# Optimization experiments

Measured on AMD Instinct MI355X. Metric: run time of the kernel, lower is better.

The kernel has to match this reference:

```python
import jax, jax.numpy as jnp
import numpy as np

NUM_SPLITS = 4
SPLIT_CH = 4          # 16 channels / 4 splits
N_BRANCH = NUM_SPLITS * 2   # 2 pyramid branches per group
K = 2                 # multi_frequency_compression k
MAX_U, MAX_V = 5, 5
N_CLASSES = 60
LN_EPS = 1e-5


def _conv(x, w):
    # x: [B, Cin, H, W], w: [Cout, Cin, kh, kw], SAME padding, stride 1
    return jax.lax.conv_general_dilated(
        x, w, window_strides=(1, 1), padding='SAME',
        dimension_numbers=('NCHW', 'OIHW', 'NCHW'))


def _branch(x, w3, b3, w5, b5, w7, b7):
    # one PyramidMultiScaleCNN branch: dense 3x3 -> 5x5 -> 7x7 with input re-concat
    a = jax.nn.relu(_conv(x, w3) + b3[None, :, None, None])            # [B,64,H,W]
    b = jax.nn.relu(_conv(jnp.concatenate([a, x], 1), w5) + b5[None, :, None, None])  # [B,128,H,W]
    c = jax.nn.relu(_conv(jnp.concatenate([b, x], 1), w7) + b7[None, :, None, None])  # [B,256,H,W]
    return jnp.concatenate([a, b, c], axis=1)                          # [B,448,H,W]


def _dct_basis(H, W, dtype):
    # first K frequency pairs (u,v) in row-major order of a MAX_U x MAX_V grid
    uv = [(i // MAX_V, i % MAX_V) for i in range(K)]
    u = jnp.array([p[0] for p in uv], dtype=dtype)   # [K]
    v = jnp.array([p[1] for p in uv], dtype=dtype)   # [K]
    h = jnp.arange(H, dtype=dtype) + 0.5
    w = jnp.arange(W, dtype=dtype) + 0.5
    cos_u = jnp.cos(jnp.pi * u[:, None] * h[None, :] / H)  # [K,H]
    cos_v = jnp.cos(jnp.pi * v[:, None] * w[None, :] / W)  # [K,W]
    return cos_u, cos_v


def setup_inputs() -> dict:
    key = jax.random.key(0)
    ks = jax.random.split(key, 16)
    B, C, H, W = 16, 16, 32, 32
    s = 0.02
    x = jax.random.normal(ks[0], (B, C, H, W), jnp.float32)
    # stacked params for the 8 identical-shaped pyramid branches (index = 2*group + branch)
    w3 = jax.random.normal(ks[1], (N_BRANCH, 64, SPLIT_CH, 3, 3), jnp.float32) * s
    b3 = jnp.zeros((N_BRANCH, 64), jnp.float32)
    w5 = jax.random.normal(ks[2], (N_BRANCH, 128, 64 + SPLIT_CH, 5, 5), jnp.float32) * s
    b5 = jnp.zeros((N_BRANCH, 128), jnp.float32)
    w7 = jax.random.normal(ks[3], (N_BRANCH, 256, 128 + SPLIT_CH, 7, 7), jnp.float32) * s
    b7 = jnp.zeros((N_BRANCH, 256), jnp.float32)
    fused_c = N_BRANCH * 448  # 3584
    Wg = jax.random.normal(ks[4], (N_CLASSES, fused_c), jnp.float32) * s
    bg = jnp.zeros((N_CLASSES,), jnp.float32)
    f_dct = fused_c * K       # 7168
    gamma = jnp.ones((f_dct,), jnp.float32)
    beta = jnp.zeros((f_dct,), jnp.float32)
    Wd = jax.random.normal(ks[5], (N_CLASSES, f_dct), jnp.float32) * s
    bd = jnp.zeros((N_CLASSES,), jnp.float32)
    return {"x": x, "w3": w3, "b3": b3, "w5": w5, "b5": b5, "w7": w7, "b7": b7,
            "Wg": Wg, "bg": bg, "gamma": gamma, "beta": beta, "Wd": Wd, "bd": bd}


def reference(x, w3, b3, w5, b5, w7, b7, Wg, bg, gamma, beta, Wd, bd):
    B, C, H, W = x.shape
    # split channels into groups: [NUM_SPLITS, B, SPLIT_CH, H, W]
    parts = x.reshape(B, NUM_SPLITS, SPLIT_CH, H, W).transpose(1, 0, 2, 3, 4)
    # each group feeds 2 branches; branch index i = 2*group + branch matches fused cat order
    xg = jnp.repeat(parts, 2, axis=0)                               # [8,B,SPLIT_CH,H,W]
    outs = jax.vmap(_branch)(xg, w3, b3, w5, b5, w7, b7)            # [8,B,448,H,W]
    fused = outs.transpose(1, 0, 2, 3, 4).reshape(B, N_BRANCH * 448, H, W)  # [B,3584,H,W]

    # GAP head
    gap_feat = fused.mean(axis=(2, 3))                              # [B,3584]
    gap_pred = gap_feat @ Wg.T + bg                                 # [B,60]

    # batched multi-frequency DCT compression (replaces per-sample Python loop)
    cos_u, cos_v = _dct_basis(H, W, fused.dtype)                    # [K,H],[K,W]
    dct = jnp.einsum('bchw,kh,kw->bck', fused, cos_u, cos_v)        # [B,3584,K]
    dct = dct.reshape(B, -1)                                        # [B,7168]

    mu = dct.mean(axis=-1, keepdims=True)
    var = jnp.var(dct, axis=-1, keepdims=True)
    normed = (dct - mu) * jax.lax.rsqrt(var + LN_EPS) * gamma + beta
    # dropout omitted (eval mode)
    dct_pred = normed @ Wd.T + bd                                   # [B,60]
    return (gap_pred, dct_pred)
```

## Files before the change

kernel.cpp:

```cpp
#include <hip/hip_runtime.h>
#include <math.h>

#define PI_F 3.14159265358979323846f

typedef short bf16x8 __attribute__((ext_vector_type(8)));
typedef float f32x4  __attribute__((ext_vector_type(4)));
typedef float f32x16 __attribute__((ext_vector_type(16)));

__device__ __forceinline__ short f2bf(float f) {
    union { float f; unsigned u; } v; v.f = f;
    unsigned r = v.u + 0x7fffu + ((v.u >> 16) & 1u);
    return (short)(r >> 16);
}

__device__ __forceinline__ void gld16(const short* g, short* l) {
    __builtin_amdgcn_global_load_lds(
        (const __attribute__((address_space(1))) unsigned int*)g,
        (__attribute__((address_space(3))) unsigned int*)l, 16, 0, 0);
}


__global__ __launch_bounds__(256) void prep_s1in(const float* __restrict__ x, short* __restrict__ dst) {
    int idx = blockIdx.x * 256 + threadIdx.x;
    if (idx >= 64 * 1024) return;
    int px = idx & 1023;
    int g  = (idx >> 10) & 3;
    int b  = idx >> 12;
    short v8[8];
    #pragma unroll
    for (int j = 0; j < 8; ++j) {
        float f = (j < 4) ? x[((b * 16 + g * 4 + j) << 10) + px] : 0.f;
        v8[j] = f2bf(f);
    }
    *(int4*)(dst + (size_t)idx * 8) = *(const int4*)v8;
}

__global__ __launch_bounds__(256) void prep_sx(const float* __restrict__ x, short* __restrict__ dst,
                                               int CHS, int CH0) {
    int idx = blockIdx.x * 256 + threadIdx.x;
    if (idx >= 128 * 1024) return;
    int px = idx & 1023, pair = idx >> 10;
    int i = pair >> 4, b = pair & 15, g = i >> 1;
    short v8[8];
    #pragma unroll
    for (int j = 0; j < 8; ++j) {
        float f = (j < 4) ? x[((b * 16 + g * 4 + j) << 10) + px] : 0.f;
        v8[j] = f2bf(f);
    }
    *(int4*)(dst + (size_t)idx * CHS + CH0) = *(const int4*)v8;
}

__global__ __launch_bounds__(256) void prep_s3x(const float* __restrict__ x, short* __restrict__ dst) {
    int idx = blockIdx.x * 256 + threadIdx.x;
    if (idx >= 128 * 1024) return;
    int px = idx & 1023, pair = idx >> 10;
    int i = pair >> 4, b = pair & 15, g = i >> 1;
    int R = px >> 5, C = px & 31;
    short v8[8];
    #pragma unroll
    for (int j = 0; j < 8; ++j) {
        float f = (j < 4) ? x[((b * 16 + g * 4 + j) << 10) + px] : 0.f;
        v8[j] = f2bf(f);
    }
    int p = ((C + 3) * 136 + 128) * 2;
    p ^= ((p >> 7) & 1) << 4;
    *(int4*)((char*)dst + ((size_t)pair * 38 + R + 3) * 11264 + p) = *(const int4*)v8;
}

template<int KS, int CHS, int CINR, int COUT, int NCH>
__global__ __launch_bounds__(256) void wprep_d(const float* __restrict__ w, short* __restrict__ Bw) {
    constexpr int TOTAL = 8 * KS * NCH * COUT * 4;
    int idx = blockIdx.x * 256 + threadIdx.x;
    if (idx >= TOTAL) return;
    int kb = idx & 3;
    int r  = idx >> 2;
    int n  = r % COUT;  r /= COUT;
    int c  = r % NCH;   r /= NCH;
    int kh = r % KS;
    int br = r / KS;
    short v8[8];
    #pragma unroll
    for (int j = 0; j < 8; ++j) {
        int k   = c * 32 + kb * 8 + j;
        int kwc = k / CHS;
        int ch  = k - kwc * CHS;
        float f = (kwc < KS && ch < CINR)
                ? w[(((size_t)br * COUT + n) * CINR + ch) * (KS * KS) + kh * KS + kwc] : 0.f;
        v8[j] = f2bf(f);
    }
    *(int4*)(Bw + (size_t)idx * 8) = *(const int4*)v8;
}

__global__ __launch_bounds__(256) void wprep7c(const float* __restrict__ w, short* __restrict__ Bw) {
    __shared__ float lds[12936];
    const int t = threadIdx.x;
    const int pairN = blockIdx.x & 127;
    const int br    = blockIdx.x >> 7;
    const int n0 = pairN * 2;
    const float* src = w + ((size_t)br * 256 + n0) * 6468;
    for (int e = t; e < 3234; e += 256)
        *(float4*)(lds + e * 4) = *(const float4*)(src + e * 4);
    __syncthreads();
    for (int e = t; e < 1680; e += 256) {
        int oct = e & 3;
        int r = e >> 2;
        int c  = r % 30; r /= 30;
        int kh = r % 7;
        int dn = r / 7;
        short v8[8];
        #pragma unroll
        for (int j = 0; j < 8; ++j) {
            int k = c * 32 + oct * 8 + j;
            int kwc = k / 136, ch = k - kwc * 136;
            float f = (kwc < 7 && ch < 132) ? lds[dn * 6468 + ch * 49 + kh * 7 + kwc] : 0.f;
            v8[j] = f2bf(f);
        }
        size_t dst = ((((size_t)br * 7 + kh) * 30 + c) * 256 + (n0 + dn)) * 32 + oct * 8;
        *(int4*)(Bw + dst) = *(const int4*)v8;
    }
}

template<int KS, int CHS, int COUT, int CHS_OUT, int FOFF, bool S1SRC, bool POUT>
__global__ __launch_bounds__(512, 2) void conv_hk(
    const short* __restrict__ sIn,
    short* __restrict__ sOut,
    const short* __restrict__ Bw,
    const float* __restrict__ bias,
    float* __restrict__ sums)
{
    constexpr int PAD    = KS / 2;
    constexpr int NCH    = (KS * CHS + 31) / 32;
    constexpr int TCX    = 32 + (NCH * 32 - 1) / CHS;
    constexpr int NSLOT  = 9;
    constexpr int NFN    = COUT / 64;
    constexpr int CPP    = CHS / 8;
    constexpr int RCHK   = TCX * CPP;
    constexpr int CHUNKB = COUT * 32;
    static_assert(NCH == 1 || (NCH % 2) == 0, "NCH must be 1 or even");
    static_assert(RCHK <= 512, "single stg reg");

    __shared__ int4 AtileV[(NSLOT * TCX * CHS) / 8];
    short* Atile = (short*)AtileV;

    const int t    = threadIdx.x;
    const int lane = t & 63, w = t >> 6;
    const int wm = w >> 2, wn = w & 3;
    const int lm = lane & 15, kb = lane >> 4;

    const int bid = blockIdx.x;
    const int i  = bid & 7;
    const int b  = (bid >> 3) & 15;
    const int mt = bid >> 7;
    const int r0 = mt * 8;

    const int pairIdx = i * 16 + b;
    const int pairPx = pairIdx << 10;
    const int srcPx  = S1SRC ? ((b * 4 + (i >> 1)) << 10) : pairPx;

    int nIdx[NFN], nOff[NFN];
    #pragma unroll
    for (int fn = 0; fn < NFN; ++fn) {
        nIdx[fn] = wn * (COUT / 4) + fn * 16 + lm;
        nOff[fn] = nIdx[fn] * 32 + kb * 8;
    }

    f32x4 acc[8][NFN];
    #pragma unroll
    for (int fm = 0; fm < 8; ++fm)
        #pragma unroll
        for (int fn = 0; fn < NFN; ++fn)
            acc[fm][fn] = (f32x4){0.f, 0.f, 0.f, 0.f};

    const short* Bp = Bw + (size_t)i * KS * NCH * CHUNKB;
    bf16x8 b0[NFN], b1[NFN];
    #pragma unroll
    for (int fn = 0; fn < NFN; ++fn)
        b0[fn] = *(const bf16x8*)(Bp + nOff[fn]);

    for (int e = t; e < 9 * RCHK; e += 512) {
        int j  = e / RCHK, e2 = e - j * RCHK;
        int tc = e2 / CPP, kc = e2 - tc * CPP;
        int rin = r0 - PAD + j, cin = tc - PAD;
        int4 v = {0, 0, 0, 0};
        if (rin >= 0 && rin < 32 && cin >= 0 && cin < 32)
            v = *(const int4*)(sIn + (size_t)(srcPx + rin * 32 + cin) * CHS + kc * 8);
        *(int4*)(Atile + (j * TCX + tc) * CHS + kc * 8) = v;
    }
    __syncthreads();

    int aB[8];

    for (int kh = 0; kh < KS; ++kh) {
        #pragma unroll
        for (int fm = 0; fm < 8; ++fm) {
            int slot = kh + wm * 4 + (fm >> 1);
            if (slot >= NSLOT) slot -= NSLOT;
            aB[fm] = (slot * TCX + (fm & 1) * 16 + lm) * CHS + kb * 8;
        }

        const bool doStage = (kh <= KS - 3);
        const int stRin = r0 - PAD + kh + 9;
        int4 stg0 = {0, 0, 0, 0};
        if (doStage) {
            if (t < RCHK) {
                int tc = t / CPP, kc = t - tc * CPP;
                int cin = tc - PAD;
                if (stRin >= 0 && stRin < 32 && cin >= 0 && cin < 32)
                    stg0 = *(const int4*)(sIn + (size_t)(srcPx + stRin * 32 + cin) * CHS + kc * 8);
            }
        }

        if constexpr (NCH == 1) {
            __builtin_amdgcn_s_setprio(1);
            #pragma unroll
            for (int fm = 0; fm < 8; ++fm) {
                bf16x8 af = *(const bf16x8*)(Atile + aB[fm]);
                #pragma unroll
                for (int fn = 0; fn < NFN; ++fn)
                    acc[fm][fn] = __builtin_amdgcn_mfma_f32_16x16x32_bf16(af, b0[fn], acc[fm][fn], 0, 0, 0);
            }
            __builtin_amdgcn_s_setprio(0);
            if (kh < KS - 1) {
                #pragma unroll
                for (int fn = 0; fn < NFN; ++fn)
                    b0[fn] = *(const bf16x8*)(Bp + CHUNKB + nOff[fn]);
            }
            Bp += CHUNKB;
        } else {
            #pragma unroll 1
            for (int c = 0; c < NCH; c += 2) {
                #pragma unroll
                for (int fn = 0; fn < NFN; ++fn)
                    b1[fn] = *(const bf16x8*)(Bp + (size_t)(c + 1) * CHUNKB + nOff[fn]);
                __builtin_amdgcn_s_setprio(1);
                #pragma unroll
                for (int fm = 0; fm < 8; ++fm) {
                    bf16x8 af = *(const bf16x8*)(Atile + aB[fm] + c * 32);
                    #pragma unroll
                    for (int fn = 0; fn < NFN; ++fn)
                        acc[fm][fn] = __builtin_amdgcn_mfma_f32_16x16x32_bf16(af, b0[fn], acc[fm][fn], 0, 0, 0);
                }
                __builtin_amdgcn_s_setprio(0);
                if (!(kh == KS - 1 && c + 2 >= NCH)) {
                    #pragma unroll
                    for (int fn = 0; fn < NFN; ++fn)
                        b0[fn] = *(const bf16x8*)(Bp + (size_t)(c + 2) * CHUNKB + nOff[fn]);
                }
                __builtin_amdgcn_s_setprio(1);
                #pragma unroll
                for (int fm = 0; fm < 8; ++fm) {
                    bf16x8 af = *(const bf16x8*)(Atile + aB[fm] + (c + 1) * 32);
                    #pragma unroll
                    for (int fn = 0; fn < NFN; ++fn)
                        acc[fm][fn] = __builtin_amdgcn_mfma_f32_16x16x32_bf16(af, b1[fn], acc[fm][fn], 0, 0, 0);
                }
                __builtin_amdgcn_s_setprio(0);
            }
            Bp += (size_t)NCH * CHUNKB;
        }

        __syncthreads();
        if (doStage && t < RCHK) {
            int tc = t / CPP, kc = t - tc * CPP;
            *(int4*)(Atile + (kh * TCX + tc) * CHS + kc * 8) = stg0;
        }
    }

    float cwv[2][4];
    #pragma unroll
    for (int half = 0; half < 2; ++half)
        #pragma unroll
        for (int r = 0; r < 4; ++r)
            cwv[half][r] = cosf(PI_F * (half * 16 + kb * 4 + r + 0.5f) / 32.f);

    #pragma unroll
    for (int fn = 0; fn < NFN; ++fn) {
        int n = nIdx[fn];
        float bv = bias[i * COUT + n];
        float s0 = 0.f, s1 = 0.f;
        #pragma unroll
        for (int fm = 0; fm < 8; ++fm) {
            int imgrow = wm * 4 + (fm >> 1);
            int half = fm & 1;
            #pragma unroll
            for (int r = 0; r < 4; ++r) {
                float v = fmaxf(acc[fm][fn][r] + bv, 0.f);
                int col = half * 16 + kb * 4 + r;
                int R = r0 + imgrow;
                if constexpr (POUT) {
                    int p = ((col + 3) * CHS_OUT + n) * 2;
                    p ^= ((p >> 7) & 1) << 4;
                    *(short*)((char*)sOut + ((size_t)pairIdx * 38 + R + 3) * 11264 + p) = f2bf(v);
                } else if constexpr (CHS_OUT > 0) {
                    sOut[(size_t)(pairPx + R * 32 + col) * CHS_OUT + n] = f2bf(v);
                }
                s0 += v;
                s1 += v * cwv[half][r];
            }
        }
        s0 += __shfl_xor(s0, 16); s1 += __shfl_xor(s1, 16);
        s0 += __shfl_xor(s0, 32); s1 += __shfl_xor(s1, 32);
        if (kb == 0) {
            int ch = i * 448 + FOFF + n;
            atomicAdd(&sums[((size_t)b * 3584 + ch) * 2 + 0], s0);
            atomicAdd(&sums[((size_t)b * 3584 + ch) * 2 + 1], s1);
        }
    }
}

__global__ __launch_bounds__(512, 2) void conv7_fused(
    const short* __restrict__ sPad,
    const short* __restrict__ Bw,
    const float* __restrict__ bias,
    float* __restrict__ sums)
{
    constexpr int NCH = 30, COUT = 256;
    constexpr int RSTR = 5632;
    constexpr int CHUNKB = COUT * 32;

    __shared__ int4 AldsV[(14 * RSTR) / 8];
    short* Alds = (short*)AldsV;

    const int t    = threadIdx.x;
    const int lane = t & 63, w = t >> 6;
    const int ln = lane & 31, hi = lane >> 5;

    const int bid = blockIdx.x;
    const int i  = bid & 7;
    const int b  = (bid >> 3) & 15;
    const int mt = bid >> 7;
    const int r0 = mt * 8;
    const size_t sBase = (size_t)(i * 16 + b) * 38 * RSTR;

    const int n = w * 32 + ln;
    const int nOffB = n * 32 + hi * 8;
    const int cstart = (w & 4) ? 15 : 0;

    f32x16 acc[8];
    #pragma unroll
    for (int ro = 0; ro < 8; ++ro) acc[ro] = (f32x16)(0.f);

    const short* BpI = Bw + (size_t)i * 7 * NCH * CHUNKB;

    for (int s = w; s < 154; s += 8) {
        int j = s / 11, sg = s - j * 11;
        gld16(sPad + sBase + (size_t)(r0 + j) * RSTR + sg * 512 + lane * 8,
              Alds + j * RSTR + sg * 512 + lane * 8);
    }
    bf16x8 bA[7], bB[7];
    #pragma unroll
    for (int kh = 0; kh < 7; ++kh)
        bA[kh] = *(const bf16x8*)(BpI + ((size_t)kh * NCH + cstart) * CHUNKB + nOffB);
    __syncthreads();

    auto HALF = [&](bf16x8 (&bq)[7], int c, int kk) {
        int swb = ln * 272 + c * 64 + kk * 32 + hi * 16;
        swb ^= ((swb >> 7) & 1) << 4;
        __builtin_amdgcn_s_setprio(1);
        #pragma unroll
        for (int j = 0; j < 14; ++j) {
            bf16x8 af = *(const bf16x8*)((const char*)Alds + j * 11264 + swb);
            const int klo = (j > 7) ? (j - 7) : 0;
            const int khi = (j < 6) ? j : 6;
            #pragma unroll
            for (int kh = klo; kh <= khi; ++kh)
                acc[j - kh] = __builtin_amdgcn_mfma_f32_32x32x16_bf16(af, bq[kh], acc[j - kh], 0, 0, 0);
        }
        __builtin_amdgcn_s_setprio(0);
    };

    #pragma unroll 1
    for (int ci = 0; ci < NCH; ++ci) {
        int cc = cstart + ci; if (cc >= NCH) cc -= NCH;
        int cn = cc + 1;      if (cn >= NCH) cn -= NCH;
        #pragma unroll
        for (int kh = 0; kh < 7; ++kh)
            bB[kh] = *(const bf16x8*)(BpI + ((size_t)kh * NCH + cc) * CHUNKB + nOffB + 16);
        HALF(bA, cc, 0);
        if (ci + 1 < NCH) {
            #pragma unroll
            for (int kh = 0; kh < 7; ++kh)
                bA[kh] = *(const bf16x8*)(BpI + ((size_t)kh * NCH + cn) * CHUNKB + nOffB);
        }
        HALF(bB, cc, 1);
    }

    float cw[16];
    #pragma unroll
    for (int r = 0; r < 16; ++r) {
        int px = (r & 3) + 8 * (r >> 2) + 4 * hi;
        cw[r] = cosf(PI_F * (px + 0.5f) / 32.f);
    }

    float bv = bias[i * COUT + n];
    float s0 = 0.f, s1 = 0.f;
    #pragma unroll
    for (int ro = 0; ro < 8; ++ro) {
        #pragma unroll
        for (int r = 0; r < 16; ++r) {
            float v = fmaxf(acc[ro][r] + bv, 0.f);
            s0 += v;
            s1 += v * cw[r];
        }
    }
    s0 += __shfl_xor(s0, 32);
    s1 += __shfl_xor(s1, 32);
    if (hi == 0) {
        int ch = i * 448 + 192 + n;
        atomicAdd(&sums[((size_t)b * 3584 + ch) * 2 + 0], s0);
        atomicAdd(&sums[((size_t)b * 3584 + ch) * 2 + 1], s1);
    }
}

__global__ __launch_bounds__(256) void ln_stats(const float* __restrict__ sums,
                                                float* __restrict__ stats) {
    __shared__ float red[8];
    const int b = blockIdx.x;
    const int t = threadIdx.x, lane = t & 63, wv = t >> 6;
    const float* S = sums + (size_t)b * 7168;
    float ls = 0.f, lq = 0.f;
    for (int f = t; f < 7168; f += 256) { float v = S[f]; ls += v; lq += v * v; }
    for (int m = 1; m < 64; m <<= 1) { ls += __shfl_xor(ls, m); lq += __shfl_xor(lq, m); }
    if (lane == 0) { red[wv] = ls; red[4 + wv] = lq; }
    __syncthreads();
    if (t == 0) {
        float ts = red[0] + red[1] + red[2] + red[3];
        float tq = red[4] + red[5] + red[6] + red[7];
        float mu  = ts * (1.f / 7168.f);
        float var = tq * (1.f / 7168.f) - mu * mu;
        stats[b * 2 + 0] = mu;
        stats[b * 2 + 1] = rsqrtf(var + 1e-5f);
    }
}

__global__ __launch_bounds__(256) void head_gemv(
    const float* __restrict__ sums,
    const float* __restrict__ stats,
    const float* __restrict__ Wg, const float* __restrict__ bg,
    const float* __restrict__ gamma, const float* __restrict__ beta,
    const float* __restrict__ Wd, const float* __restrict__ bd,
    float* __restrict__ out)
{
    __shared__ float red[8];
    const int n = blockIdx.x % 60;
    const int b = blockIdx.x / 60;
    const int t = threadIdx.x, lane = t & 63, wv = t >> 6;
    const float* S  = sums + (size_t)b * 7168;
    const float mu  = stats[b * 2 + 0];
    const float inv = stats[b * 2 + 1];

    const float* wd = Wd + (size_t)n * 7168;
    float accd = 0.f;
    for (int f = t; f < 7168; f += 256) {
        float v = (S[f] - mu) * inv * gamma[f] + beta[f];
        accd = fmaf(v, wd[f], accd);
    }
    const float* wg = Wg + (size_t)n * 3584;
    float accg = 0.f;
    for (int ch = t; ch < 3584; ch += 256)
        accg = fmaf(S[2 * ch], wg[ch], accg);

    for (int m = 1; m < 64; m <<= 1) { accg += __shfl_xor(accg, m); accd += __shfl_xor(accd, m); }
    if (lane == 0) { red[wv] = accg; red[4 + wv] = accd; }
    __syncthreads();
    if (t == 0) {
        float g = red[0] + red[1] + red[2] + red[3];
        float d = red[4] + red[5] + red[6] + red[7];
        out[b * 60 + n]       = g * (1.f / 1024.f) + bg[n];
        out[960 + b * 60 + n] = d + bd[n];
    }
}

extern "C" void kernel_launch(void* const* d_in, const int* in_sizes, int n_in,
                              void* d_out, int out_size, void* d_ws, size_t ws_size,
                              hipStream_t stream)
{
    const float* x     = (const float*)d_in[0];
    const float* w3    = (const float*)d_in[1];
    const float* b3    = (const float*)d_in[2];
    const float* w5    = (const float*)d_in[3];
    const float* b5    = (const float*)d_in[4];
    const float* w7    = (const float*)d_in[5];
    const float* b7    = (const float*)d_in[6];
    const float* Wg    = (const float*)d_in[7];
    const float* bg    = (const float*)d_in[8];
    const float* gamma = (const float*)d_in[9];
    const float* beta  = (const float*)d_in[10];
    const float* Wd    = (const float*)d_in[11];
    const float* bd    = (const float*)d_in[12];
    float* out = (float*)d_out;

    char* p = (char*)d_ws;
    float* sums  = (float*)p;             p += 458752;
    float* stats = (float*)p;             p += 128;
    short* s1in  = (short*)p;             p += 1048576;
    short* s2in  = (short*)p;             p += 18874368;
    short* s3pad = (short*)p;             p += 54788096;
    short* Bw3   = (short*)p;             p += 98304;
    short* Bw5   = (short*)p;             p += 3932160;
    short* Bw7   = (short*)p;             p += 27525120;

    hipMemsetAsync(sums, 0, 458752, stream);
    hipMemsetAsync(s3pad, 0, 54788096, stream);
    prep_s1in<<<dim3(256), dim3(256), 0, stream>>>(x, s1in);
    prep_sx<<<dim3(512), dim3(256), 0, stream>>>(x, s2in, 72, 64);
    prep_s3x<<<dim3(512), dim3(256), 0, stream>>>(x, s3pad);
    wprep_d<3, 8, 4, 64, 1><<<dim3(24), dim3(256), 0, stream>>>(w3, Bw3);
    wprep_d<5, 72, 68, 128, 12><<<dim3(960), dim3(256), 0, stream>>>(w5, Bw5);
    wprep7c<<<dim3(1024), dim3(256), 0, stream>>>(w7, Bw7);

    conv_hk<3, 8, 64, 72, 0, true, false><<<dim3(512), dim3(512), 0, stream>>>(s1in, s2in, Bw3, b3, sums);
    conv_hk<5, 72, 128, 136, 64, false, true><<<dim3(512), dim3(512), 0, stream>>>(s2in, s3pad, Bw5, b5, sums);
    conv7_fused<<<dim3(512), dim3(512), 0, stream>>>(s3pad, Bw7, b7, sums);

    ln_stats<<<dim3(16), dim3(256), 0, stream>>>(sums, stats);
    head_gemv<<<dim3(960), dim3(256), 0, stream>>>(sums, stats, Wg, bg, gamma, beta, Wd, bd, out);
}
```

Before: 449.9 us.

## Merge all prep kernels and memsets into one block-dispatched launch

Replaces two memsets and six separate prep/weight-repack kernels with a single mega_prep kernel that dispatches on block index ranges. The full 54MB memset of s3pad is replaced by zeroing only the halo rows and the padding columns not written by later stages. This removes launch overhead and a large amount of redundant memory write traffic. The risk is that any padding region missed by the selective zeroing would leave stale data. Every block now also reserves the large shared-memory array, which may limit occupancy for the simple blocks.

```diff
diff --git a/kernel.cpp b/kernel.cpp
--- a/kernel.cpp
+++ b/kernel.cpp
@@ -19,59 +19,8 @@
         (__attribute__((address_space(3))) unsigned int*)l, 16, 0, 0);
 }
 
-
-__global__ __launch_bounds__(256) void prep_s1in(const float* __restrict__ x, short* __restrict__ dst) {
-    int idx = blockIdx.x * 256 + threadIdx.x;
-    if (idx >= 64 * 1024) return;
-    int px = idx & 1023;
-    int g  = (idx >> 10) & 3;
-    int b  = idx >> 12;
-    short v8[8];
-    #pragma unroll
-    for (int j = 0; j < 8; ++j) {
-        float f = (j < 4) ? x[((b * 16 + g * 4 + j) << 10) + px] : 0.f;
-        v8[j] = f2bf(f);
-    }
-    *(int4*)(dst + (size_t)idx * 8) = *(const int4*)v8;
-}
-
-__global__ __launch_bounds__(256) void prep_sx(const float* __restrict__ x, short* __restrict__ dst,
-                                               int CHS, int CH0) {
-    int idx = blockIdx.x * 256 + threadIdx.x;
-    if (idx >= 128 * 1024) return;
-    int px = idx & 1023, pair = idx >> 10;
-    int i = pair >> 4, b = pair & 15, g = i >> 1;
-    short v8[8];
-    #pragma unroll
-    for (int j = 0; j < 8; ++j) {
-        float f = (j < 4) ? x[((b * 16 + g * 4 + j) << 10) + px] : 0.f;
-        v8[j] = f2bf(f);
-    }
-    *(int4*)(dst + (size_t)idx * CHS + CH0) = *(const int4*)v8;
-}
-
-__global__ __launch_bounds__(256) void prep_s3x(const float* __restrict__ x, short* __restrict__ dst) {
-    int idx = blockIdx.x * 256 + threadIdx.x;
-    if (idx >= 128 * 1024) return;
-    int px = idx & 1023, pair = idx >> 10;
-    int i = pair >> 4, b = pair & 15, g = i >> 1;
-    int R = px >> 5, C = px & 31;
-    short v8[8];
-    #pragma unroll
-    for (int j = 0; j < 8; ++j) {
-        float f = (j < 4) ? x[((b * 16 + g * 4 + j) << 10) + px] : 0.f;
-        v8[j] = f2bf(f);
-    }
-    int p = ((C + 3) * 136 + 128) * 2;
-    p ^= ((p >> 7) & 1) << 4;
-    *(int4*)((char*)dst + ((size_t)pair * 38 + R + 3) * 11264 + p) = *(const int4*)v8;
-}
-
-template<int KS, int CHS, int CINR, int COUT, int NCH>
-__global__ __launch_bounds__(256) void wprep_d(const float* __restrict__ w, short* __restrict__ Bw) {
-    constexpr int TOTAL = 8 * KS * NCH * COUT * 4;
-    int idx = blockIdx.x * 256 + threadIdx.x;
-    if (idx >= TOTAL) return;
+__device__ __forceinline__ void wprep_body(const float* __restrict__ w, short* __restrict__ Bw,
+                                           int idx, int KS, int CHS, int CINR, int COUT, int NCH) {
     int kb = idx & 3;
     int r  = idx >> 2;
     int n  = r % COUT;  r /= COUT;
@@ -91,32 +40,124 @@
     *(int4*)(Bw + (size_t)idx * 8) = *(const int4*)v8;
 }
 
-__global__ __launch_bounds__(256) void wprep7c(const float* __restrict__ w, short* __restrict__ Bw) {
+__global__ __launch_bounds__(256) void mega_prep(
+    const float* __restrict__ x,  const float* __restrict__ w3,
+    const float* __restrict__ w5, const float* __restrict__ w7,
+    float* __restrict__ sums, short* __restrict__ s1in, short* __restrict__ s2in,
+    short* __restrict__ s3pad, short* __restrict__ Bw3, short* __restrict__ Bw5,
+    short* __restrict__ Bw7)
+{
     __shared__ float lds[12936];
+    int blk = blockIdx.x;
     const int t = threadIdx.x;
-    const int pairN = blockIdx.x & 127;
-    const int br    = blockIdx.x >> 7;
-    const int n0 = pairN * 2;
-    const float* src = w + ((size_t)br * 256 + n0) * 6468;
-    for (int e = t; e < 3234; e += 256)
-        *(float4*)(lds + e * 4) = *(const float4*)(src + e * 4);
-    __syncthreads();
-    for (int e = t; e < 1680; e += 256) {
-        int oct = e & 3;
-        int r = e >> 2;
-        int c  = r % 30; r /= 30;
-        int kh = r % 7;
-        int dn = r / 7;
+
+    if (blk < 112) {
+        int idx = blk * 256 + t;
+        *(float4*)((char*)sums + (size_t)idx * 16) = (float4){0.f, 0.f, 0.f, 0.f};
+        return;
+    }
+    blk -= 112;
+    if (blk < 128) {
+        char* base = (char*)s3pad + (size_t)blk * 38 * 11264;
+        const int4 z = {0, 0, 0, 0};
+        for (int e = t; e < 6 * 704; e += 256) {
+            int rj = e / 704, ch = e - rj * 704;
+            int row = (rj < 3) ? rj : (32 + rj);
+            *(int4*)(base + (size_t)row * 11264 + ch * 16) = z;
+        }
+        for (int e = t; e < 32 * 160; e += 256) {
+            int row = 3 + e / 160, k = e % 160;
+            size_t rb = (size_t)row * 11264;
+            if (k < 51)       *(int4*)(base + rb + k * 16) = z;
+            else if (k < 102) *(int4*)(base + rb + 9520 + (k - 51) * 16) = z;
+            else              *(int4*)(base + rb + 10336 + (k - 102) * 16) = z;
+        }
+        return;
+    }
+    blk -= 128;
+    if (blk < 256) {
+        int idx = blk * 256 + t;
+        int px = idx & 1023;
+        int g  = (idx >> 10) & 3;
+        int b  = idx >> 12;
         short v8[8];
         #pragma unroll
         for (int j = 0; j < 8; ++j) {
-            int k = c * 32 + oct * 8 + j;
-            int kwc = k / 136, ch = k - kwc * 136;
-            float f = (kwc < 7 && ch < 132) ? lds[dn * 6468 + ch * 49 + kh * 7 + kwc] : 0.f;
+            float f = (j < 4) ? x[((b * 16 + g * 4 + j) << 10) + px] : 0.f;
             v8[j] = f2bf(f);
         }
-        size_t dst = ((((size_t)br * 7 + kh) * 30 + c) * 256 + (n0 + dn)) * 32 + oct * 8;
-        *(int4*)(Bw + dst) = *(const int4*)v8;
+        *(int4*)(s1in + (size_t)idx * 8) = *(const int4*)v8;
+        return;
+    }
+    blk -= 256;
+    if (blk < 512) {
+        int idx = blk * 256 + t;
+        int px = idx & 1023, pair = idx >> 10;
+        int i = pair >> 4, b = pair & 15, g = i >> 1;
+        short v8[8];
+        #pragma unroll
+        for (int j = 0; j < 8; ++j) {
+            float f = (j < 4) ? x[((b * 16 + g * 4 + j) << 10) + px] : 0.f;
+            v8[j] = f2bf(f);
+        }
+        *(int4*)(s2in + (size_t)idx * 72 + 64) = *(const int4*)v8;
+        return;
+    }
+    blk -= 512;
+    if (blk < 512) {
+        int idx = blk * 256 + t;
+        int px = idx & 1023, pair = idx >> 10;
+        int i = pair >> 4, b = pair & 15, g = i >> 1;
+        int R = px >> 5, C = px & 31;
+        short v8[8];
+        #pragma unroll
+        for (int j = 0; j < 8; ++j) {
+            float f = (j < 4) ? x[((b * 16 + g * 4 + j) << 10) + px] : 0.f;
+            v8[j] = f2bf(f);
+        }
+        int p = ((C + 3) * 136 + 128) * 2;
+        p ^= ((p >> 7) & 1) << 4;
+        *(int4*)((char*)s3pad + ((size_t)pair * 38 + R + 3) * 11264 + p) = *(const int4*)v8;
+        return;
+    }
+    blk -= 512;
+    if (blk < 24) {
+        int idx = blk * 256 + t;
+        wprep_body(w3, Bw3, idx, 3, 8, 4, 64, 1);
+        return;
+    }
+    blk -= 24;
+    if (blk < 960) {
+        int idx = blk * 256 + t;
+        wprep_body(w5, Bw5, idx, 5, 72, 68, 128, 12);
+        return;
+    }
+    blk -= 960;
+    {
+        const int pairN = blk & 127;
+        const int br    = blk >> 7;
+        const int n0 = pairN * 2;
+        const float* src = w7 + ((size_t)br * 256 + n0) * 6468;
+        for (int e = t; e < 3234; e += 256)
+            *(float4*)(lds + e * 4) = *(const float4*)(src + e * 4);
+        __syncthreads();
+        for (int e = t; e < 1680; e += 256) {
+            int oct = e & 3;
+            int r = e >> 2;
+            int c  = r % 30; r /= 30;
+            int kh = r % 7;
+            int dn = r / 7;
+            short v8[8];
+            #pragma unroll
+            for (int j = 0; j < 8; ++j) {
+                int k = c * 32 + oct * 8 + j;
+                int kwc = k / 136, ch = k - kwc * 136;
+                float f = (kwc < 7 && ch < 132) ? lds[dn * 6468 + ch * 49 + kh * 7 + kwc] : 0.f;
+                v8[j] = f2bf(f);
+            }
+            size_t dst = ((((size_t)br * 7 + kh) * 30 + c) * 256 + (n0 + dn)) * 32 + oct * 8;
+            *(int4*)(Bw7 + dst) = *(const int4*)v8;
+        }
     }
 }
 
@@ -500,14 +541,8 @@
     short* Bw5   = (short*)p;             p += 3932160;
     short* Bw7   = (short*)p;             p += 27525120;
 
-    hipMemsetAsync(sums, 0, 458752, stream);
-    hipMemsetAsync(s3pad, 0, 54788096, stream);
-    prep_s1in<<<dim3(256), dim3(256), 0, stream>>>(x, s1in);
-    prep_sx<<<dim3(512), dim3(256), 0, stream>>>(x, s2in, 72, 64);
-    prep_s3x<<<dim3(512), dim3(256), 0, stream>>>(x, s3pad);
-    wprep_d<3, 8, 4, 64, 1><<<dim3(24), dim3(256), 0, stream>>>(w3, Bw3);
-    wprep_d<5, 72, 68, 128, 12><<<dim3(960), dim3(256), 0, stream>>>(w5, Bw5);
-    wprep7c<<<dim3(1024), dim3(256), 0, stream>>>(w7, Bw7);
+    mega_prep<<<dim3(3528), dim3(256), 0, stream>>>(x, w3, w5, w7,
+        sums, s1in, s2in, s3pad, Bw3, Bw5, Bw7);
 
     conv_hk<3, 8, 64, 72, 0, true, false><<<dim3(512), dim3(512), 0, stream>>>(s1in, s2in, Bw3, b3, sums);
     conv_hk<5, 72, 128, 136, 64, false, true><<<dim3(512), dim3(512), 0, stream>>>(s2in, s3pad, Bw5, b5, sums);
```

After: 425.1 us. 5.5% less time.
